# Kernel tuning notes

Hardware: AMD Instinct MI355X
Metric: run time of the kernel (lower is better)

The kernel has to match this reference:

```python
import jax, jax.numpy as jnp
import numpy as np

NUM_SRC = 200000
NUM_DST = 100000
NUM_EDGES = 1600000
IN_DIM = 128
HID = 256
OUT_DIM = 128


def layer_norm(h, g, b, eps=1e-5):
    mu = jnp.mean(h, axis=-1, keepdims=True)
    var = jnp.mean((h - mu) ** 2, axis=-1, keepdims=True)
    return (h - mu) * jax.lax.rsqrt(var + eps) * g + b


def setup_inputs() -> dict:
    key = jax.random.key(0)
    ks = jax.random.split(key, 8)
    s_in = 1.0 / np.sqrt(IN_DIM)
    s_hid = 1.0 / np.sqrt(HID)
    return {
        "x": jax.random.normal(ks[0], (NUM_SRC, IN_DIM), dtype=jnp.float32),
        "w_l": jax.random.normal(ks[1], (IN_DIM, HID), dtype=jnp.float32) * s_in,
        "b_l": jnp.zeros((HID,), dtype=jnp.float32),
        "w_r": jax.random.normal(ks[2], (IN_DIM, HID), dtype=jnp.float32) * s_in,
        "ln1_g": jnp.ones((HID,), dtype=jnp.float32),
        "ln1_b": jnp.zeros((HID,), dtype=jnp.float32),
        "w_out": jax.random.normal(ks[3], (HID, OUT_DIM), dtype=jnp.float32) * s_hid,
        "b_out": jnp.zeros((OUT_DIM,), dtype=jnp.float32),
        "ln2_g": jnp.ones((OUT_DIM,), dtype=jnp.float32),
        "ln2_b": jnp.zeros((OUT_DIM,), dtype=jnp.float32),
        "edge_src": jax.random.randint(ks[4], (NUM_EDGES,), 0, NUM_SRC, dtype=jnp.int64),
        "edge_dst": jax.random.randint(ks[5], (NUM_EDGES,), 0, NUM_DST, dtype=jnp.int64),
    }


def reference(x, w_l, b_l, w_r, ln1_g, ln1_b, w_out, b_out, ln2_g, ln2_b, edge_src, edge_dst):
    # SAGEConv bipartite: targets are the first NUM_DST rows of x
    x_tgt = x[:NUM_DST]
    # mean aggregation of source-node messages at destination nodes
    msgs = x[edge_src]  # [E, IN_DIM] irregular gather
    summed = jax.ops.segment_sum(msgs, edge_dst, num_segments=NUM_DST)
    cnt = jax.ops.segment_sum(jnp.ones((NUM_EDGES,), dtype=x.dtype), edge_dst, num_segments=NUM_DST)
    mean_nbr = summed / jnp.maximum(cnt, 1.0)[:, None]
    # out = lin_l(aggr) + lin_r(x_target); dropout p=0 is identity
    h = mean_nbr @ w_l + b_l + x_tgt @ w_r
    h = layer_norm(h, ln1_g, ln1_b)
    h = jax.nn.gelu(h, approximate=False)
    out = h @ w_out + b_out
    out = layer_norm(out, ln2_g, ln2_b)
    return out
```

## Files before the change

### kernel.cpp

```cpp
#include <hip/hip_runtime.h>
#include <math.h>

#define NSRC 200000
#define NDST 100000
#define NEDGE 1600000

typedef unsigned int uint32;
typedef unsigned short u16;

typedef short short8 __attribute__((ext_vector_type(8)));
typedef float f32x4 __attribute__((ext_vector_type(4)));

__device__ __forceinline__ u16 f2b(float f) {
  uint32 u = __float_as_uint(f);
  u += 0x7fffu + ((u >> 16) & 1u);
  return (u16)(u >> 16);
}
__device__ __forceinline__ float b2f_lo(uint32 u) { return __uint_as_float(u << 16); }
__device__ __forceinline__ float b2f_hi(uint32 u) { return __uint_as_float(u & 0xffff0000u); }

__global__ void k_cvt_prepack(const float* __restrict__ x, u16* __restrict__ xb,
                              const float* __restrict__ wl, const float* __restrict__ wr,
                              const float* __restrict__ wo, u16* __restrict__ wp1f,
                              u16* __restrict__ wp2f, const int do_cvt) {
  if (blockIdx.x < 384) {
    int t = blockIdx.x * 256 + threadIdx.x;
    if (t < 65536) {
      int j = t & 7, lane = (t >> 3) & 63, nt = (t >> 9) & 3, kc = (t >> 11) & 7, w = t >> 14;
      int k = kc * 32 + (lane >> 4) * 8 + j;
      int n = w * 64 + nt * 16 + (lane & 15);
      float v = (k < 128) ? wl[k * 256 + n] : wr[(k - 128) * 256 + n];
      wp1f[t] = f2b(v);
    } else {
      int t2 = t - 65536;
      int j = t2 & 7, lane = (t2 >> 3) & 63, nt = (t2 >> 9) & 1, kc = (t2 >> 10) & 7, w = t2 >> 13;
      int k = kc * 32 + (lane >> 4) * 8 + j;
      int n = w * 32 + nt * 16 + (lane & 15);
      wp2f[t2] = f2b(wo[k * 128 + n]);
    }
    return;
  }
  if (!do_cvt) return;
  int idx = (blockIdx.x - 384) * 256 + threadIdx.x;
  size_t i = (size_t)idx * 4;
  if (i < (size_t)NSRC * 128) {
    float4 f = *(const float4*)(x + i);
    uint2 o;
    o.x = (uint32)f2b(f.x) | ((uint32)f2b(f.y) << 16);
    o.y = (uint32)f2b(f.z) | ((uint32)f2b(f.w) << 16);
    *(uint2*)(xb + i) = o;
  }
}

#define BCHUNK 2048

__global__ __launch_bounds__(256) void k_bucket_direct(const int* __restrict__ src,
                                                       const int* __restrict__ dst,
                                                       int* __restrict__ cnt,
                                                       int* __restrict__ csr,
                                                       const int cap) {
  __shared__ int sd[BCHUNK], ss[BCHUNK];
  int base = blockIdx.x * BCHUNK;
  for (int i = threadIdx.x; i < BCHUNK; i += 256) {
    int e = base + i;
    sd[i] = (e < NEDGE) ? dst[e] : -1;
    ss[i] = (e < NEDGE) ? src[e] : 0;
  }
  __syncthreads();
  for (int p = 0; p < 8; p++) {
    int lo = p * 12500;
    int hi = lo + 12500;
    for (int i = threadIdx.x; i < BCHUNK; i += 256) {
      int d = sd[i];
      if (d >= lo && d < hi) {
        int pos = atomicAdd(&cnt[d], 1);
        if (pos < cap) csr[(size_t)d * cap + pos] = ss[i];
      }
    }
  }
}

__global__ __launch_bounds__(256) void k_agg_bf16(const u16* __restrict__ xb,
                                                  const int* __restrict__ csr,
                                                  const int* __restrict__ cnt,
                                                  u16* __restrict__ meanb, const int cap) {
  int d = blockIdx.x * 16 + (threadIdx.x >> 4);
  int sub = threadIdx.x & 15;
  if (d >= NDST) return;
  int n = cnt[d];
  int m = n < cap ? n : cap;
  const int* cp = csr + (size_t)d * cap;
  float a[8] = {0, 0, 0, 0, 0, 0, 0, 0};
  int i = 0;
  for (; i + 3 < m; i += 4) {
    int s0 = cp[i];
    int s1 = cp[i + 1];
    int s2 = cp[i + 2];
    int s3 = cp[i + 3];
    uint4 p0 = *(const uint4*)(xb + (size_t)s0 * 128 + sub * 8);
    uint4 p1 = *(const uint4*)(xb + (size_t)s1 * 128 + sub * 8);
    uint4 p2 = *(const uint4*)(xb + (size_t)s2 * 128 + sub * 8);
    uint4 p3 = *(const uint4*)(xb + (size_t)s3 * 128 + sub * 8);
    a[0] += b2f_lo(p0.x); a[1] += b2f_hi(p0.x);
    a[2] += b2f_lo(p0.y); a[3] += b2f_hi(p0.y);
    a[4] += b2f_lo(p0.z); a[5] += b2f_hi(p0.z);
    a[6] += b2f_lo(p0.w); a[7] += b2f_hi(p0.w);
    a[0] += b2f_lo(p1.x); a[1] += b2f_hi(p1.x);
    a[2] += b2f_lo(p1.y); a[3] += b2f_hi(p1.y);
    a[4] += b2f_lo(p1.z); a[5] += b2f_hi(p1.z);
    a[6] += b2f_lo(p1.w); a[7] += b2f_hi(p1.w);
    a[0] += b2f_lo(p2.x); a[1] += b2f_hi(p2.x);
    a[2] += b2f_lo(p2.y); a[3] += b2f_hi(p2.y);
    a[4] += b2f_lo(p2.z); a[5] += b2f_hi(p2.z);
    a[6] += b2f_lo(p2.w); a[7] += b2f_hi(p2.w);
    a[0] += b2f_lo(p3.x); a[1] += b2f_hi(p3.x);
    a[2] += b2f_lo(p3.y); a[3] += b2f_hi(p3.y);
    a[4] += b2f_lo(p3.z); a[5] += b2f_hi(p3.z);
    a[6] += b2f_lo(p3.w); a[7] += b2f_hi(p3.w);
  }
  for (; i < m; i++) {
    int s0 = cp[i];
    uint4 p = *(const uint4*)(xb + (size_t)s0 * 128 + sub * 8);
    a[0] += b2f_lo(p.x); a[1] += b2f_hi(p.x);
    a[2] += b2f_lo(p.y); a[3] += b2f_hi(p.y);
    a[4] += b2f_lo(p.z); a[5] += b2f_hi(p.z);
    a[6] += b2f_lo(p.w); a[7] += b2f_hi(p.w);
  }
  float sc = 1.f / (float)(n > 0 ? n : 1);
  uint4 o;
  o.x = (uint32)f2b(a[0] * sc) | ((uint32)f2b(a[1] * sc) << 16);
  o.y = (uint32)f2b(a[2] * sc) | ((uint32)f2b(a[3] * sc) << 16);
  o.z = (uint32)f2b(a[4] * sc) | ((uint32)f2b(a[5] * sc) << 16);
  o.w = (uint32)f2b(a[6] * sc) | ((uint32)f2b(a[7] * sc) << 16);
  *(uint4*)(meanb + (size_t)d * 128 + sub * 8) = o;
}

__global__ __launch_bounds__(256) void k_agg_f32(const float* __restrict__ x,
                                                 const int* __restrict__ csr,
                                                 const int* __restrict__ cnt,
                                                 u16* __restrict__ meanb, const int cap) {
  int d = blockIdx.x * 16 + (threadIdx.x >> 4);
  int sub = threadIdx.x & 15;
  if (d >= NDST) return;
  int n = cnt[d];
  int m = n < cap ? n : cap;
  const int* cp = csr + (size_t)d * cap;
  float a[8] = {0, 0, 0, 0, 0, 0, 0, 0};
  for (int i = 0; i < m; i++) {
    int s = cp[i];
    const float* p = x + (size_t)s * 128 + sub * 8;
    float4 f0 = *(const float4*)p;
    float4 f1 = *(const float4*)(p + 4);
    a[0] += f0.x; a[1] += f0.y; a[2] += f0.z; a[3] += f0.w;
    a[4] += f1.x; a[5] += f1.y; a[6] += f1.z; a[7] += f1.w;
  }
  float sc = 1.f / (float)(n > 0 ? n : 1);
  uint4 o;
  o.x = (uint32)f2b(a[0] * sc) | ((uint32)f2b(a[1] * sc) << 16);
  o.y = (uint32)f2b(a[2] * sc) | ((uint32)f2b(a[3] * sc) << 16);
  o.z = (uint32)f2b(a[4] * sc) | ((uint32)f2b(a[5] * sc) << 16);
  o.w = (uint32)f2b(a[6] * sc) | ((uint32)f2b(a[7] * sc) << 16);
  *(uint4*)(meanb + (size_t)d * 128 + sub * 8) = o;
}

#define LDAH 264

__global__ __launch_bounds__(256) void k_fused(
    const u16* __restrict__ meanb, const u16* __restrict__ xb, const float* __restrict__ xf,
    const int x_is_bf16, const u16* __restrict__ wp1f, const u16* __restrict__ wp2f,
    const float* __restrict__ bl_g, const float* __restrict__ g1_g, const float* __restrict__ b1_g,
    const float* __restrict__ bo_g, const float* __restrict__ g2_g, const float* __restrict__ b2_g,
    float* __restrict__ out) {
  __shared__ __align__(16) u16 AH_lds[64 * LDAH];
  __shared__ float2 stats[4][64];
  __shared__ float2 stats2[64];

  const int tid = threadIdx.x;
  const int wave = tid >> 6;
  const int lane = tid & 63;
  const int l15 = lane & 15;
  const int q = lane >> 4;
  const int row0 = blockIdx.x * 64;

  {
    int arow = tid >> 2;
    int c4 = tid & 3;
    int aR = row0 + arow;
    uint4* dm = (uint4*)(AH_lds + arow * LDAH);
    uint4* dx = dm + 16;
    if (aR < NDST) {
      const uint4* mp = (const uint4*)(meanb + (size_t)aR * 128);
#pragma unroll
      for (int i = 0; i < 4; i++) dm[c4 + 4 * i] = mp[c4 + 4 * i];
      if (x_is_bf16) {
        const uint4* xp = (const uint4*)(xb + (size_t)aR * 128);
#pragma unroll
        for (int i = 0; i < 4; i++) dx[c4 + 4 * i] = xp[c4 + 4 * i];
      } else {
        const float* p = xf + (size_t)aR * 128;
#pragma unroll
        for (int i = 0; i < 4; i++) {
          int j = c4 + 4 * i;
          float4 f0 = *(const float4*)(p + j * 8);
          float4 f1 = *(const float4*)(p + j * 8 + 4);
          uint4 v;
          v.x = (uint32)f2b(f0.x) | ((uint32)f2b(f0.y) << 16);
          v.y = (uint32)f2b(f0.z) | ((uint32)f2b(f0.w) << 16);
          v.z = (uint32)f2b(f1.x) | ((uint32)f2b(f1.y) << 16);
          v.w = (uint32)f2b(f1.z) | ((uint32)f2b(f1.w) << 16);
          dx[j] = v;
        }
      }
    } else {
      uint4 z = {0u, 0u, 0u, 0u};
#pragma unroll
      for (int i = 0; i < 4; i++) { dm[c4 + 4 * i] = z; dx[c4 + 4 * i] = z; }
    }
  }
  __syncthreads();

  f32x4 acc[4][4];
#pragma unroll
  for (int i = 0; i < 4; i++)
#pragma unroll
    for (int j = 0; j < 4; j++) acc[i][j] = (f32x4){0.f, 0.f, 0.f, 0.f};

#pragma unroll 2
  for (int kc = 0; kc < 8; kc++) {
    short8 bfr[4];
    const uint4* bsrc = (const uint4*)(wp1f + (((size_t)wave * 8 + kc) * 4) * 512);
#pragma unroll
    for (int nt = 0; nt < 4; nt++) bfr[nt] = ((const short8*)(bsrc + nt * 64))[lane];
    short8 af[4];
#pragma unroll
    for (int mt = 0; mt < 4; mt++)
      af[mt] = *(const short8*)(AH_lds + (16 * mt + l15) * LDAH + kc * 32 + q * 8);
#pragma unroll
    for (int mt = 0; mt < 4; mt++)
#pragma unroll
      for (int nt = 0; nt < 4; nt++)
        acc[mt][nt] = __builtin_amdgcn_mfma_f32_16x16x32_bf16(af[mt], bfr[nt], acc[mt][nt], 0, 0, 0);
  }

  float bl[4], g1[4], b1[4];
#pragma unroll
  for (int nt = 0; nt < 4; nt++) {
    int c = 64 * wave + 16 * nt + l15;
    bl[nt] = bl_g[c]; g1[nt] = g1_g[c]; b1[nt] = b1_g[c];
  }
#pragma unroll
  for (int mt = 0; mt < 4; mt++)
#pragma unroll
    for (int nt = 0; nt < 4; nt++)
#pragma unroll
      for (int r = 0; r < 4; r++) acc[mt][nt][r] += bl[nt];

#pragma unroll
  for (int mt = 0; mt < 4; mt++)
#pragma unroll
    for (int r = 0; r < 4; r++) {
      float s = 0.f, s2 = 0.f;
#pragma unroll
      for (int nt = 0; nt < 4; nt++) { float v = acc[mt][nt][r]; s += v; s2 += v * v; }
#pragma unroll
      for (int m = 1; m < 16; m <<= 1) { s += __shfl_xor(s, m, 64); s2 += __shfl_xor(s2, m, 64); }
      if (l15 == 0) stats[wave][16 * mt + 4 * q + r] = make_float2(s, s2);
    }
  __syncthreads();
  if (tid < 64) {
    float S = 0.f, Q = 0.f;
#pragma unroll
    for (int w = 0; w < 4; w++) { float2 t = stats[w][tid]; S += t.x; Q += t.y; }
    float mu = S * (1.f / 256.f);
    float var = Q * (1.f / 256.f) - mu * mu;
    stats2[tid] = make_float2(mu, rsqrtf(var + 1e-5f));
  }
  __syncthreads();
#pragma unroll
  for (int mt = 0; mt < 4; mt++)
#pragma unroll
    for (int r = 0; r < 4; r++) {
      int row = 16 * mt + 4 * q + r;
      float2 st = stats2[row];
#pragma unroll
      for (int nt = 0; nt < 4; nt++) {
        float v = acc[mt][nt][r];
        float hn = (v - st.x) * st.y * g1[nt] + b1[nt];
        float t2 = hn * hn;
        float u = fmaf(0.044715f * t2, hn, hn);
        float ge = hn / (1.f + __expf(-1.5957691216f * u));
        AH_lds[row * LDAH + 64 * wave + 16 * nt + l15] = f2b(ge);
      }
    }
  __syncthreads();

  f32x4 acc2[4][2];
#pragma unroll
  for (int i = 0; i < 4; i++)
#pragma unroll
    for (int j = 0; j < 2; j++) acc2[i][j] = (f32x4){0.f, 0.f, 0.f, 0.f};

#pragma unroll 2
  for (int kc = 0; kc < 8; kc++) {
    short8 bfr[2];
    const uint4* bsrc = (const uint4*)(wp2f + (((size_t)wave * 8 + kc) * 2) * 512);
#pragma unroll
    for (int nt = 0; nt < 2; nt++) bfr[nt] = ((const short8*)(bsrc + nt * 64))[lane];
    short8 af[4];
#pragma unroll
    for (int mt = 0; mt < 4; mt++)
      af[mt] = *(const short8*)(AH_lds + (16 * mt + l15) * LDAH + kc * 32 + q * 8);
#pragma unroll
    for (int mt = 0; mt < 4; mt++)
#pragma unroll
      for (int nt = 0; nt < 2; nt++)
        acc2[mt][nt] = __builtin_amdgcn_mfma_f32_16x16x32_bf16(af[mt], bfr[nt], acc2[mt][nt], 0, 0, 0);
  }

  float bo[2], g2[2], b2c[2];
#pragma unroll
  for (int nt = 0; nt < 2; nt++) {
    int c = 32 * wave + 16 * nt + l15;
    bo[nt] = bo_g[c]; g2[nt] = g2_g[c]; b2c[nt] = b2_g[c];
  }
#pragma unroll
  for (int mt = 0; mt < 4; mt++)
#pragma unroll
    for (int nt = 0; nt < 2; nt++)
#pragma unroll
      for (int r = 0; r < 4; r++) acc2[mt][nt][r] += bo[nt];

#pragma unroll
  for (int mt = 0; mt < 4; mt++)
#pragma unroll
    for (int r = 0; r < 4; r++) {
      float s = 0.f, s2 = 0.f;
#pragma unroll
      for (int nt = 0; nt < 2; nt++) { float v = acc2[mt][nt][r]; s += v; s2 += v * v; }
#pragma unroll
      for (int m = 1; m < 16; m <<= 1) { s += __shfl_xor(s, m, 64); s2 += __shfl_xor(s2, m, 64); }
      if (l15 == 0) stats[wave][16 * mt + 4 * q + r] = make_float2(s, s2);
    }
  __syncthreads();
  if (tid < 64) {
    float S = 0.f, Q = 0.f;
#pragma unroll
    for (int w = 0; w < 4; w++) { float2 t = stats[w][tid]; S += t.x; Q += t.y; }
    float mu = S * (1.f / 128.f);
    float var = Q * (1.f / 128.f) - mu * mu;
    stats2[tid] = make_float2(mu, rsqrtf(var + 1e-5f));
  }
  __syncthreads();
#pragma unroll
  for (int mt = 0; mt < 4; mt++)
#pragma unroll
    for (int r = 0; r < 4; r++) {
      int row = 16 * mt + 4 * q + r;
      int R = row0 + row;
      if (R < NDST) {
        float2 st = stats2[row];
#pragma unroll
        for (int nt = 0; nt < 2; nt++) {
          float v = acc2[mt][nt][r];
          out[(size_t)R * 128 + 32 * wave + 16 * nt + l15] = (v - st.x) * st.y * g2[nt] + b2c[nt];
        }
      }
    }
}

extern "C" void kernel_launch(void* const* d_in, const int* in_sizes, int n_in,
                              void* d_out, int out_size, void* d_ws, size_t ws_size,
                              hipStream_t stream) {
  const float* x   = (const float*)d_in[0];
  const float* w_l = (const float*)d_in[1];
  const float* b_l = (const float*)d_in[2];
  const float* w_r = (const float*)d_in[3];
  const float* g1  = (const float*)d_in[4];
  const float* b1  = (const float*)d_in[5];
  const float* w_o = (const float*)d_in[6];
  const float* b_o = (const float*)d_in[7];
  const float* g2  = (const float*)d_in[8];
  const float* b2  = (const float*)d_in[9];
  const int* esrc  = (const int*)d_in[10];
  const int* edst  = (const int*)d_in[11];
  float* out = (float*)d_out;

  char* ws = (char*)d_ws;
  size_t off = 0;
  auto alloc = [&](size_t bytes) -> void* {
    off = (off + 255) & ~(size_t)255;
    void* p = ws + off;
    off += bytes;
    return p;
  };
  int* cnt   = (int*)alloc((size_t)NDST * 4);
  u16* wp1f  = (u16*)alloc((size_t)65536 * 2);
  u16* wp2f  = (u16*)alloc((size_t)32768 * 2);
  u16* meanb = (u16*)alloc((size_t)NDST * 128 * 2);

  size_t rem = (ws_size > off + 512) ? (ws_size - off - 512) : 0;
  size_t xb_bytes = (size_t)NSRC * 128 * 2;
  int cap;
  int x_is_bf16;
  if (rem >= (size_t)NDST * 64 * 4 + xb_bytes) { cap = 64; x_is_bf16 = 1; }
  else if (rem >= (size_t)NDST * 64 * 4)       { cap = 64; x_is_bf16 = 0; }
  else if (rem >= (size_t)NDST * 32 * 4)       { cap = 32; x_is_bf16 = 0; }
  else                                         { cap = 16; x_is_bf16 = 0; }
  int* csr = (int*)alloc((size_t)NDST * cap * 4);
  u16* xb = x_is_bf16 ? (u16*)alloc(xb_bytes) : nullptr;

  hipMemsetAsync(cnt, 0, (size_t)NDST * 4, stream);
  k_cvt_prepack<<<384 + 25000, 256, 0, stream>>>(x, xb, w_l, w_r, w_o, wp1f, wp2f, x_is_bf16);
  k_bucket_direct<<<(NEDGE + BCHUNK - 1) / BCHUNK, 256, 0, stream>>>(esrc, edst, cnt, csr, cap);
  if (x_is_bf16)
    k_agg_bf16<<<(NDST + 15) / 16, 256, 0, stream>>>(xb, csr, cnt, meanb, cap);
  else
    k_agg_f32<<<(NDST + 15) / 16, 256, 0, stream>>>(x, csr, cnt, meanb, cap);
  k_fused<<<(NDST + 63) / 64, 256, 0, stream>>>(meanb, xb, x, x_is_bf16, wp1f, wp2f,
                                                b_l, g1, b1, b_o, g2, b2, out);
}
```

Baseline: 414.5 us.

## Fuse neighbor aggregation into GEMM kernel and merge prepack with bucketing

The mean-aggregation gather now runs inside the fused MLP kernel, so each block builds its mean rows directly in LDS and the bf16 meanb round trip through global memory goes away. The conversion/prepack kernel and the edge bucketing kernel become one launch, split by block index. Together this cuts two kernel launches and the intermediate write and read. The risk is lower occupancy or latency hiding in the fused kernel, since its gather phase is irregular and runs before the MFMA work in the same block.

```diff
diff --git a/kernel.cpp b/kernel.cpp
--- a/kernel.cpp
+++ b/kernel.cpp
@@ -19,10 +19,16 @@
 __device__ __forceinline__ float b2f_lo(uint32 u) { return __uint_as_float(u << 16); }
 __device__ __forceinline__ float b2f_hi(uint32 u) { return __uint_as_float(u & 0xffff0000u); }
 
-__global__ void k_cvt_prepack(const float* __restrict__ x, u16* __restrict__ xb,
-                              const float* __restrict__ wl, const float* __restrict__ wr,
-                              const float* __restrict__ wo, u16* __restrict__ wp1f,
-                              u16* __restrict__ wp2f, const int do_cvt) {
+#define BCHUNK 2048
+#define NBUCKET ((NEDGE + BCHUNK - 1) / BCHUNK)
+
+__global__ __launch_bounds__(256) void k_combo(
+    const float* __restrict__ x, u16* __restrict__ xb,
+    const float* __restrict__ wl, const float* __restrict__ wr, const float* __restrict__ wo,
+    u16* __restrict__ wp1f, u16* __restrict__ wp2f,
+    const int* __restrict__ esrc, const int* __restrict__ edst,
+    int* __restrict__ cnt, int* __restrict__ csr, const int cap, const int do_cvt) {
+  __shared__ int sd[BCHUNK], ss[BCHUNK];
   if (blockIdx.x < 384) {
     int t = blockIdx.x * 256 + threadIdx.x;
     if (t < 65536) {
@@ -40,31 +46,24 @@
     }
     return;
   }
-  if (!do_cvt) return;
-  int idx = (blockIdx.x - 384) * 256 + threadIdx.x;
-  size_t i = (size_t)idx * 4;
-  if (i < (size_t)NSRC * 128) {
-    float4 f = *(const float4*)(x + i);
-    uint2 o;
-    o.x = (uint32)f2b(f.x) | ((uint32)f2b(f.y) << 16);
-    o.y = (uint32)f2b(f.z) | ((uint32)f2b(f.w) << 16);
-    *(uint2*)(xb + i) = o;
-  }
-}
-
-#define BCHUNK 2048
-
-__global__ __launch_bounds__(256) void k_bucket_direct(const int* __restrict__ src,
-                                                       const int* __restrict__ dst,
-                                                       int* __restrict__ cnt,
-                                                       int* __restrict__ csr,
-                                                       const int cap) {
-  __shared__ int sd[BCHUNK], ss[BCHUNK];
-  int base = blockIdx.x * BCHUNK;
+  if (blockIdx.x < 384 + 25000) {
+    if (!do_cvt) return;
+    int idx = (blockIdx.x - 384) * 256 + threadIdx.x;
+    size_t i = (size_t)idx * 4;
+    if (i < (size_t)NSRC * 128) {
+      float4 f = *(const float4*)(x + i);
+      uint2 o;
+      o.x = (uint32)f2b(f.x) | ((uint32)f2b(f.y) << 16);
+      o.y = (uint32)f2b(f.z) | ((uint32)f2b(f.w) << 16);
+      *(uint2*)(xb + i) = o;
+    }
+    return;
+  }
+  int base = (blockIdx.x - (384 + 25000)) * BCHUNK;
   for (int i = threadIdx.x; i < BCHUNK; i += 256) {
     int e = base + i;
-    sd[i] = (e < NEDGE) ? dst[e] : -1;
-    ss[i] = (e < NEDGE) ? src[e] : 0;
+    sd[i] = (e < NEDGE) ? edst[e] : -1;
+    ss[i] = (e < NEDGE) ? esrc[e] : 0;
   }
   __syncthreads();
   for (int p = 0; p < 8; p++) {
@@ -80,94 +79,12 @@
   }
 }
 
-__global__ __launch_bounds__(256) void k_agg_bf16(const u16* __restrict__ xb,
-                                                  const int* __restrict__ csr,
-                                                  const int* __restrict__ cnt,
-                                                  u16* __restrict__ meanb, const int cap) {
-  int d = blockIdx.x * 16 + (threadIdx.x >> 4);
-  int sub = threadIdx.x & 15;
-  if (d >= NDST) return;
-  int n = cnt[d];
-  int m = n < cap ? n : cap;
-  const int* cp = csr + (size_t)d * cap;
-  float a[8] = {0, 0, 0, 0, 0, 0, 0, 0};
-  int i = 0;
-  for (; i + 3 < m; i += 4) {
-    int s0 = cp[i];
-    int s1 = cp[i + 1];
-    int s2 = cp[i + 2];
-    int s3 = cp[i + 3];
-    uint4 p0 = *(const uint4*)(xb + (size_t)s0 * 128 + sub * 8);
-    uint4 p1 = *(const uint4*)(xb + (size_t)s1 * 128 + sub * 8);
-    uint4 p2 = *(const uint4*)(xb + (size_t)s2 * 128 + sub * 8);
-    uint4 p3 = *(const uint4*)(xb + (size_t)s3 * 128 + sub * 8);
-    a[0] += b2f_lo(p0.x); a[1] += b2f_hi(p0.x);
-    a[2] += b2f_lo(p0.y); a[3] += b2f_hi(p0.y);
-    a[4] += b2f_lo(p0.z); a[5] += b2f_hi(p0.z);
-    a[6] += b2f_lo(p0.w); a[7] += b2f_hi(p0.w);
-    a[0] += b2f_lo(p1.x); a[1] += b2f_hi(p1.x);
-    a[2] += b2f_lo(p1.y); a[3] += b2f_hi(p1.y);
-    a[4] += b2f_lo(p1.z); a[5] += b2f_hi(p1.z);
-    a[6] += b2f_lo(p1.w); a[7] += b2f_hi(p1.w);
-    a[0] += b2f_lo(p2.x); a[1] += b2f_hi(p2.x);
-    a[2] += b2f_lo(p2.y); a[3] += b2f_hi(p2.y);
-    a[4] += b2f_lo(p2.z); a[5] += b2f_hi(p2.z);
-    a[6] += b2f_lo(p2.w); a[7] += b2f_hi(p2.w);
-    a[0] += b2f_lo(p3.x); a[1] += b2f_hi(p3.x);
-    a[2] += b2f_lo(p3.y); a[3] += b2f_hi(p3.y);
-    a[4] += b2f_lo(p3.z); a[5] += b2f_hi(p3.z);
-    a[6] += b2f_lo(p3.w); a[7] += b2f_hi(p3.w);
-  }
-  for (; i < m; i++) {
-    int s0 = cp[i];
-    uint4 p = *(const uint4*)(xb + (size_t)s0 * 128 + sub * 8);
-    a[0] += b2f_lo(p.x); a[1] += b2f_hi(p.x);
-    a[2] += b2f_lo(p.y); a[3] += b2f_hi(p.y);
-    a[4] += b2f_lo(p.z); a[5] += b2f_hi(p.z);
-    a[6] += b2f_lo(p.w); a[7] += b2f_hi(p.w);
-  }
-  float sc = 1.f / (float)(n > 0 ? n : 1);
-  uint4 o;
-  o.x = (uint32)f2b(a[0] * sc) | ((uint32)f2b(a[1] * sc) << 16);
-  o.y = (uint32)f2b(a[2] * sc) | ((uint32)f2b(a[3] * sc) << 16);
-  o.z = (uint32)f2b(a[4] * sc) | ((uint32)f2b(a[5] * sc) << 16);
-  o.w = (uint32)f2b(a[6] * sc) | ((uint32)f2b(a[7] * sc) << 16);
-  *(uint4*)(meanb + (size_t)d * 128 + sub * 8) = o;
-}
-
-__global__ __launch_bounds__(256) void k_agg_f32(const float* __restrict__ x,
-                                                 const int* __restrict__ csr,
-                                                 const int* __restrict__ cnt,
-                                                 u16* __restrict__ meanb, const int cap) {
-  int d = blockIdx.x * 16 + (threadIdx.x >> 4);
-  int sub = threadIdx.x & 15;
-  if (d >= NDST) return;
-  int n = cnt[d];
-  int m = n < cap ? n : cap;
-  const int* cp = csr + (size_t)d * cap;
-  float a[8] = {0, 0, 0, 0, 0, 0, 0, 0};
-  for (int i = 0; i < m; i++) {
-    int s = cp[i];
-    const float* p = x + (size_t)s * 128 + sub * 8;
-    float4 f0 = *(const float4*)p;
-    float4 f1 = *(const float4*)(p + 4);
-    a[0] += f0.x; a[1] += f0.y; a[2] += f0.z; a[3] += f0.w;
-    a[4] += f1.x; a[5] += f1.y; a[6] += f1.z; a[7] += f1.w;
-  }
-  float sc = 1.f / (float)(n > 0 ? n : 1);
-  uint4 o;
-  o.x = (uint32)f2b(a[0] * sc) | ((uint32)f2b(a[1] * sc) << 16);
-  o.y = (uint32)f2b(a[2] * sc) | ((uint32)f2b(a[3] * sc) << 16);
-  o.z = (uint32)f2b(a[4] * sc) | ((uint32)f2b(a[5] * sc) << 16);
-  o.w = (uint32)f2b(a[6] * sc) | ((uint32)f2b(a[7] * sc) << 16);
-  *(uint4*)(meanb + (size_t)d * 128 + sub * 8) = o;
-}
-
 #define LDAH 264
 
 __global__ __launch_bounds__(256) void k_fused(
-    const u16* __restrict__ meanb, const u16* __restrict__ xb, const float* __restrict__ xf,
-    const int x_is_bf16, const u16* __restrict__ wp1f, const u16* __restrict__ wp2f,
+    const u16* __restrict__ xb, const float* __restrict__ xf, const int x_is_bf16,
+    const int* __restrict__ cnt_g, const int* __restrict__ csr, const int cap,
+    const u16* __restrict__ wp1f, const u16* __restrict__ wp2f,
     const float* __restrict__ bl_g, const float* __restrict__ g1_g, const float* __restrict__ b1_g,
     const float* __restrict__ bo_g, const float* __restrict__ g2_g, const float* __restrict__ b2_g,
     float* __restrict__ out) {
@@ -183,38 +100,84 @@
   const int row0 = blockIdx.x * 64;
 
   {
-    int arow = tid >> 2;
-    int c4 = tid & 3;
-    int aR = row0 + arow;
-    uint4* dm = (uint4*)(AH_lds + arow * LDAH);
-    uint4* dx = dm + 16;
-    if (aR < NDST) {
-      const uint4* mp = (const uint4*)(meanb + (size_t)aR * 128);
-#pragma unroll
-      for (int i = 0; i < 4; i++) dm[c4 + 4 * i] = mp[c4 + 4 * i];
-      if (x_is_bf16) {
-        const uint4* xp = (const uint4*)(xb + (size_t)aR * 128);
-#pragma unroll
-        for (int i = 0; i < 4; i++) dx[c4 + 4 * i] = xp[c4 + 4 * i];
-      } else {
-        const float* p = xf + (size_t)aR * 128;
-#pragma unroll
-        for (int i = 0; i < 4; i++) {
-          int j = c4 + 4 * i;
-          float4 f0 = *(const float4*)(p + j * 8);
-          float4 f1 = *(const float4*)(p + j * 8 + 4);
-          uint4 v;
-          v.x = (uint32)f2b(f0.x) | ((uint32)f2b(f0.y) << 16);
-          v.y = (uint32)f2b(f0.z) | ((uint32)f2b(f0.w) << 16);
-          v.z = (uint32)f2b(f1.x) | ((uint32)f2b(f1.y) << 16);
-          v.w = (uint32)f2b(f1.z) | ((uint32)f2b(f1.w) << 16);
-          dx[j] = v;
+    int rgrp = lane >> 4;
+    int sub = lane & 15;
+#pragma unroll
+    for (int g = 0; g < 4; g++) {
+      int row = wave * 16 + g * 4 + rgrp;
+      int R = row0 + row;
+      float a[8] = {0, 0, 0, 0, 0, 0, 0, 0};
+      int n = 0;
+      if (R < NDST) {
+        n = cnt_g[R];
+        int m = n < cap ? n : cap;
+        const int* cp = csr + (size_t)R * cap;
+        if (x_is_bf16) {
+          int i = 0;
+          for (; i + 3 < m; i += 4) {
+            int s0 = cp[i], s1 = cp[i + 1], s2 = cp[i + 2], s3 = cp[i + 3];
+            uint4 p0 = *(const uint4*)(xb + (size_t)s0 * 128 + sub * 8);
+            uint4 p1 = *(const uint4*)(xb + (size_t)s1 * 128 + sub * 8);
+            uint4 p2 = *(const uint4*)(xb + (size_t)s2 * 128 + sub * 8);
+            uint4 p3 = *(const uint4*)(xb + (size_t)s3 * 128 + sub * 8);
+            a[0] += b2f_lo(p0.x); a[1] += b2f_hi(p0.x);
+            a[2] += b2f_lo(p0.y); a[3] += b2f_hi(p0.y);
+            a[4] += b2f_lo(p0.z); a[5] += b2f_hi(p0.z);
+            a[6] += b2f_lo(p0.w); a[7] += b2f_hi(p0.w);
+            a[0] += b2f_lo(p1.x); a[1] += b2f_hi(p1.x);
+            a[2] += b2f_lo(p1.y); a[3] += b2f_hi(p1.y);
+            a[4] += b2f_lo(p1.z); a[5] += b2f_hi(p1.z);
+            a[6] += b2f_lo(p1.w); a[7] += b2f_hi(p1.w);
+            a[0] += b2f_lo(p2.x); a[1] += b2f_hi(p2.x);
+            a[2] += b2f_lo(p2.y); a[3] += b2f_hi(p2.y);
+            a[4] += b2f_lo(p2.z); a[5] += b2f_hi(p2.z);
+            a[6] += b2f_lo(p2.w); a[7] += b2f_hi(p2.w);
+            a[0] += b2f_lo(p3.x); a[1] += b2f_hi(p3.x);
+            a[2] += b2f_lo(p3.y); a[3] += b2f_hi(p3.y);
+            a[4] += b2f_lo(p3.z); a[5] += b2f_hi(p3.z);
+            a[6] += b2f_lo(p3.w); a[7] += b2f_hi(p3.w);
+          }
+          for (; i < m; i++) {
+            int s0 = cp[i];
+            uint4 p = *(const uint4*)(xb + (size_t)s0 * 128 + sub * 8);
+            a[0] += b2f_lo(p.x); a[1] += b2f_hi(p.x);
+            a[2] += b2f_lo(p.y); a[3] += b2f_hi(p.y);
+            a[4] += b2f_lo(p.z); a[5] += b2f_hi(p.z);
+            a[6] += b2f_lo(p.w); a[7] += b2f_hi(p.w);
+          }
+        } else {
+          for (int i = 0; i < m; i++) {
+            int s = cp[i];
+            const float* p = xf + (size_t)s * 128 + sub * 8;
+            float4 f0 = *(const float4*)p;
+            float4 f1 = *(const float4*)(p + 4);
+            a[0] += f0.x; a[1] += f0.y; a[2] += f0.z; a[3] += f0.w;
+            a[4] += f1.x; a[5] += f1.y; a[6] += f1.z; a[7] += f1.w;
+          }
         }
       }
-    } else {
-      uint4 z = {0u, 0u, 0u, 0u};
-#pragma unroll
-      for (int i = 0; i < 4; i++) { dm[c4 + 4 * i] = z; dx[c4 + 4 * i] = z; }
+      float sc = 1.f / (float)(n > 0 ? n : 1);
+      uint4 o;
+      o.x = (uint32)f2b(a[0] * sc) | ((uint32)f2b(a[1] * sc) << 16);
+      o.y = (uint32)f2b(a[2] * sc) | ((uint32)f2b(a[3] * sc) << 16);
+      o.z = (uint32)f2b(a[4] * sc) | ((uint32)f2b(a[5] * sc) << 16);
+      o.w = (uint32)f2b(a[6] * sc) | ((uint32)f2b(a[7] * sc) << 16);
+      *(uint4*)(AH_lds + row * LDAH + sub * 8) = o;
+      uint4 xv = {0u, 0u, 0u, 0u};
+      if (R < NDST) {
+        if (x_is_bf16) {
+          xv = *(const uint4*)(xb + (size_t)R * 128 + sub * 8);
+        } else {
+          const float* p = xf + (size_t)R * 128 + sub * 8;
+          float4 f0 = *(const float4*)p;
+          float4 f1 = *(const float4*)(p + 4);
+          xv.x = (uint32)f2b(f0.x) | ((uint32)f2b(f0.y) << 16);
+          xv.y = (uint32)f2b(f0.z) | ((uint32)f2b(f0.w) << 16);
+          xv.z = (uint32)f2b(f1.x) | ((uint32)f2b(f1.y) << 16);
+          xv.w = (uint32)f2b(f1.z) | ((uint32)f2b(f1.w) << 16);
+        }
+      }
+      *(uint4*)(AH_lds + row * LDAH + 128 + sub * 8) = xv;
     }
   }
   __syncthreads();
@@ -393,10 +356,9 @@
     off += bytes;
     return p;
   };
-  int* cnt   = (int*)alloc((size_t)NDST * 4);
-  u16* wp1f  = (u16*)alloc((size_t)65536 * 2);
-  u16* wp2f  = (u16*)alloc((size_t)32768 * 2);
-  u16* meanb = (u16*)alloc((size_t)NDST * 128 * 2);
+  int* cnt  = (int*)alloc((size_t)NDST * 4);
+  u16* wp1f = (u16*)alloc((size_t)65536 * 2);
+  u16* wp2f = (u16*)alloc((size_t)32768 * 2);
 
   size_t rem = (ws_size > off + 512) ? (ws_size - off - 512) : 0;
   size_t xb_bytes = (size_t)NSRC * 128 * 2;
@@ -410,12 +372,8 @@
   u16* xb = x_is_bf16 ? (u16*)alloc(xb_bytes) : nullptr;
 
   hipMemsetAsync(cnt, 0, (size_t)NDST * 4, stream);
-  k_cvt_prepack<<<384 + 25000, 256, 0, stream>>>(x, xb, w_l, w_r, w_o, wp1f, wp2f, x_is_bf16);
-  k_bucket_direct<<<(NEDGE + BCHUNK - 1) / BCHUNK, 256, 0, stream>>>(esrc, edst, cnt, csr, cap);
-  if (x_is_bf16)
-    k_agg_bf16<<<(NDST + 15) / 16, 256, 0, stream>>>(xb, csr, cnt, meanb, cap);
-  else
-    k_agg_f32<<<(NDST + 15) / 16, 256, 0, stream>>>(x, csr, cnt, meanb, cap);
-  k_fused<<<(NDST + 63) / 64, 256, 0, stream>>>(meanb, xb, x, x_is_bf16, wp1f, wp2f,
+  k_combo<<<384 + 25000 + NBUCKET, 256, 0, stream>>>(x, xb, w_l, w_r, w_o, wp1f, wp2f,
+                                                     esrc, edst, cnt, csr, cap, x_is_bf16);
+  k_fused<<<(NDST + 63) / 64, 256, 0, stream>>>(xb, x, x_is_bf16, cnt, csr, cap, wp1f, wp2f,
                                                 b_l, g1, b1, b_o, g2, b2, out);
 }
```

Measured after the change: 445.4 us. +7.4%, slower.
